# Performance work log

Measured on AMD Instinct MI355X. Metric: run time of the kernel, lower is better.

## Reference

```python
import jax, jax.numpy as jnp
import numpy as np
from jax import lax

HID, PROJ, DYN = 256, 256, 64
HW, BS, NQ = 6400, 16, 100


def setup_inputs() -> dict:
    key = jax.random.key(0)
    ks = jax.random.split(key, 10)
    p = lambda k, shape: jax.random.normal(k, shape, jnp.float32) * 0.02
    return {
        "query_feat": jax.random.normal(ks[0], (HW, BS, HID), jnp.float32),
        "support_feat": jax.random.normal(ks[1], (NQ, BS, HID), jnp.float32),
        "h": 80,
        "w": 80,
        "Wq": p(ks[2], (HID, PROJ)), "bq": jnp.zeros((PROJ,), jnp.float32),
        "Ws": p(ks[3], (HID, PROJ)), "bsp": jnp.zeros((PROJ,), jnp.float32),
        "W1": p(ks[4], (PROJ, DYN)), "b1": jnp.zeros((DYN,), jnp.float32),
        "W2": p(ks[5], (DYN, HID)), "b2": jnp.zeros((HID,), jnp.float32),
    }


def reference(query_feat, support_feat, h, w, Wq, bq, Ws, bsp, W1, b1, W2, b2):
    # query_feat: [hw, bs, c] -> [bs, hw, c]; support_feat: [nq, bs, c] -> [bs, nq, c]
    qf = jnp.transpose(query_feat, (1, 0, 2))
    sf = jnp.transpose(support_feat, (1, 0, 2))
    bsz, nq = sf.shape[0], sf.shape[1]
    hw = h * w

    fs_proj = sf @ Ws + bsp                      # [bs, nq, proj]
    fq_proj = qf @ Wq + bq                       # [bs, hw, proj]
    pattern = jnp.tanh(jax.nn.relu(fs_proj @ W1 + b1) @ W2 + b2)
    fs_feat = (pattern + 1.0) * fs_proj          # [bs, nq, proj]

    # bmm(fq, fs^T).T -> [bs, nq, hw]
    sim = jnp.einsum("bkp,bnp->bnk", fq_proj, fs_feat)
    similarity = sim.reshape(bsz, nq, h, w)

    # coordinate grid: x varies along w, y along h; flattened [hw, 2]
    gy = jnp.arange(h, dtype=jnp.float32) + 0.5
    gx = jnp.arange(w, dtype=jnp.float32) + 0.5
    X, Y = jnp.meshgrid(gx, gy, indexing="xy")  # each [h, w]
    coord = jnp.stack([X, Y], axis=-1).reshape(hw, 2)
    side = jnp.array([w, h], dtype=jnp.float32)

    sm = jax.nn.softmax(sim, axis=-1)            # [bs, nq, hw]
    proposal_for_loss = jnp.einsum("bnk,kd->bnd", sm, coord) / side

    # argmax peak -> one-hot -> 3x3 max-pool dilation (note (w,h) reshape per original)
    max_pos = jnp.argmax(sim, axis=-1)           # [bs, nq]
    max_mask = jax.nn.one_hot(max_pos, hw, dtype=jnp.float32).reshape(bsz, nq, w, h)
    local_mask = lax.reduce_window(
        max_mask, -jnp.inf, lax.max,
        window_dimensions=(1, 1, 3, 3), window_strides=(1, 1, 1, 1),
        padding=[(0, 0), (0, 0), (1, 1), (1, 1)],
    ).reshape(bsz, nq, hw)

    local_sm = sm * local_mask
    local_sm = local_sm / (jnp.sum(local_sm, axis=-1, keepdims=True) + 1e-10)
    proposals = jnp.einsum("bnk,kd->bnd", local_sm, coord) / side

    return proposal_for_loss, similarity, proposals
```

## Files before the change

kernel.cpp:

```cpp
#include <hip/hip_runtime.h>

#define HID 256
#define PROJ 256
#define DYN 64
#define HWD 6400
#define BSZ 16
#define NQ 100
#define HH 80
#define WW 80

typedef unsigned short u16;
typedef u16 u16x8 __attribute__((ext_vector_type(8)));
typedef __bf16 bf16x8 __attribute__((ext_vector_type(8)));
typedef float f32x4 __attribute__((ext_vector_type(4)));

__device__ __forceinline__ float bf2f(u16 h) {
    union { unsigned u; float f; } c; c.u = ((unsigned)h) << 16; return c.f;
}
__device__ __forceinline__ u16 f2bf(float f) {
    union { float f; unsigned u; } c; c.f = f;
    return (u16)((c.u + 0x7FFFu + ((c.u >> 16) & 1u)) >> 16);
}

__global__ __launch_bounds__(256, 1) void kpre(
    const float* __restrict__ support,
    const float* __restrict__ Wq, const float* __restrict__ bq,
    const float* __restrict__ Ws, const float* __restrict__ bsp,
    const float* __restrict__ W1, const float* __restrict__ b1,
    const float* __restrict__ W2, const float* __restrict__ b2,
    u16* __restrict__ pack, float* __restrict__ cvec)
{
    const int c = blockIdx.x;
    const int b = blockIdx.y;
    const int t = threadIdx.x;
    const int wv = t >> 6, lane = t & 63;

    __shared__ __align__(16) float sf_t[HID][8];
    __shared__ __align__(16) float fsp[8][PROJ];
    __shared__ __align__(16) float hid[8][DYN];
    __shared__ __align__(16) float fsf_t[PROJ][8];
    __shared__ float cacc[8][4];

    {
        const int nl = t >> 5;
        const int i0 = (t & 31) * 8;
        const int n = c * 8 + nl;
        float v[8];
        if (n < NQ) {
            const float* sp = support + (size_t)n * (BSZ * HID) + (size_t)b * HID + i0;
            const f32x4 a = *reinterpret_cast<const f32x4*>(sp);
            const f32x4 bb = *reinterpret_cast<const f32x4*>(sp + 4);
            v[0]=a[0]; v[1]=a[1]; v[2]=a[2]; v[3]=a[3];
            v[4]=bb[0]; v[5]=bb[1]; v[6]=bb[2]; v[7]=bb[3];
        } else {
            #pragma unroll
            for (int j = 0; j < 8; ++j) v[j] = 0.f;
        }
        #pragma unroll
        for (int j = 0; j < 8; ++j) sf_t[i0 + j][nl] = v[j];
    }
    __syncthreads();

    {
        const int p = t;
        float acc[8];
        #pragma unroll
        for (int n = 0; n < 8; ++n) acc[n] = 0.f;
        for (int i0 = 0; i0 < HID; i0 += 8) {
            float w[8];
            #pragma unroll
            for (int j = 0; j < 8; ++j) w[j] = Ws[(size_t)(i0 + j) * PROJ + p];
            #pragma unroll
            for (int j = 0; j < 8; ++j) {
                const f32x4 s0 = *reinterpret_cast<const f32x4*>(&sf_t[i0 + j][0]);
                const f32x4 s1 = *reinterpret_cast<const f32x4*>(&sf_t[i0 + j][4]);
                acc[0] += s0[0] * w[j]; acc[1] += s0[1] * w[j];
                acc[2] += s0[2] * w[j]; acc[3] += s0[3] * w[j];
                acc[4] += s1[0] * w[j]; acc[5] += s1[1] * w[j];
                acc[6] += s1[2] * w[j]; acc[7] += s1[3] * w[j];
            }
        }
        const float bb = bsp[p];
        #pragma unroll
        for (int n = 0; n < 8; ++n) fsp[n][p] = acc[n] + bb;
    }
    __syncthreads();

    {
        const int d = lane;
        #pragma unroll
        for (int pass = 0; pass < 2; ++pass) {
            const int nl = pass * 4 + wv;
            float a = 0.f;
            for (int p0 = 0; p0 < PROJ; p0 += 8) {
                float w[8];
                #pragma unroll
                for (int j = 0; j < 8; ++j) w[j] = W1[(size_t)(p0 + j) * DYN + d];
                #pragma unroll
                for (int j = 0; j < 8; ++j) a += fsp[nl][p0 + j] * w[j];
            }
            a += b1[d];
            hid[nl][d] = a > 0.f ? a : 0.f;
        }
    }
    __syncthreads();

    float cp[8];
    {
        const int p = t;
        const float bqv = bq[p];
        const float b2v = b2[p];
        float w[8][8];
        #pragma unroll
        for (int d0 = 0; d0 < 8; ++d0)
            #pragma unroll
            for (int j = 0; j < 8; ++j) w[d0][j] = W2[(size_t)(d0 * 8 + j) * PROJ + p];
        #pragma unroll
        for (int nl = 0; nl < 8; ++nl) {
            float a = 0.f;
            #pragma unroll
            for (int d0 = 0; d0 < 8; ++d0)
                #pragma unroll
                for (int j = 0; j < 8; ++j) a += hid[nl][d0 * 8 + j] * w[d0][j];
            const float pat = tanhf(a + b2v);
            const float ff = (pat + 1.f) * fsp[nl][p];
            fsf_t[p][nl] = ff;
            cp[nl] = bqv * ff;
        }
    }
    __syncthreads();

    #pragma unroll
    for (int nl = 0; nl < 8; ++nl) {
        float v = cp[nl];
        for (int off = 32; off > 0; off >>= 1) v += __shfl_down(v, off);
        if (lane == 0) cacc[nl][wv] = v;
    }
    __syncthreads();
    if (t < 8) {
        const int n = c * 8 + t;
        if (n < NQ) cvec[b * NQ + n] = cacc[t][0] + cacc[t][1] + cacc[t][2] + cacc[t][3];
    }

    {
        const int h = t;
        float acc[8];
        #pragma unroll
        for (int n = 0; n < 8; ++n) acc[n] = 0.f;
        for (int p0 = 0; p0 < PROJ; p0 += 8) {
            const float* wp = Wq + (size_t)h * PROJ + p0;
            const f32x4 w0 = *reinterpret_cast<const f32x4*>(wp);
            const f32x4 w1 = *reinterpret_cast<const f32x4*>(wp + 4);
            float wv8[8] = {w0[0], w0[1], w0[2], w0[3], w1[0], w1[1], w1[2], w1[3]};
            #pragma unroll
            for (int j = 0; j < 8; ++j) {
                const float w = wv8[j];
                const f32x4 f0 = *reinterpret_cast<const f32x4*>(&fsf_t[p0 + j][0]);
                const f32x4 f1 = *reinterpret_cast<const f32x4*>(&fsf_t[p0 + j][4]);
                acc[0] += f0[0] * w; acc[1] += f0[1] * w;
                acc[2] += f0[2] * w; acc[3] += f0[3] * w;
                acc[4] += f1[0] * w; acc[5] += f1[1] * w;
                acc[6] += f1[2] * w; acc[7] += f1[3] * w;
            }
        }
        const int ks = h >> 5, quad = (h >> 3) & 3, j = h & 7;
        const int nt = c >> 1;
        #pragma unroll
        for (int nl = 0; nl < 8; ++nl) {
            const int n = c * 8 + nl;
            const float f = (n < NQ) ? acc[nl] : 0.f;
            const u16 hi = f2bf(f);
            const u16 lo = f2bf(f - bf2f(hi));
            const int nit = (c & 1) * 8 + nl;
            const int lane2 = quad * 16 + nit;
            const size_t base = ((((size_t)b * 2 + 0) * 8 + ks) * 8 + nt) * 512 + lane2 * 8 + j;
            const size_t baseL = base + (size_t)8 * 8 * 512;
            pack[base] = hi;
            pack[baseL] = lo;
        }
    }
}

__global__ __launch_bounds__(256, 4) void ksim(
    const float* __restrict__ qf,
    const u16* __restrict__ pack,
    const float* __restrict__ cvec,
    float* __restrict__ sim)
{
    const int mc = blockIdx.x;
    const int b  = blockIdx.y;
    const int wv = threadIdx.x >> 6;
    const int lane = threadIdx.x & 63;
    const int quad = lane >> 4, l16 = lane & 15;

    f32x4 acc[7];
    #pragma unroll
    for (int nt = 0; nt < 7; ++nt) acc[nt] = (f32x4){0.f, 0.f, 0.f, 0.f};

    const int row = mc * 64 + wv * 16 + l16;
    const float* ap = qf + (size_t)row * (BSZ * HID) + b * HID + quad * 8;
    const u16* pb = pack + (size_t)b * (2 * 8 * 8 * 64 * 8) + (size_t)lane * 8;

    f32x4 a0 = *reinterpret_cast<const f32x4*>(ap + 0);
    f32x4 a1 = *reinterpret_cast<const f32x4*>(ap + 4);

    #pragma unroll
    for (int ks = 0; ks < 8; ++ks) {
        u16x8 uh[7], ul[7];
        #pragma unroll
        for (int nt = 0; nt < 7; ++nt) {
            uh[nt] = *reinterpret_cast<const u16x8*>(pb + ((size_t)(0 * 8 + ks) * 8 + nt) * 512);
            ul[nt] = *reinterpret_cast<const u16x8*>(pb + ((size_t)(1 * 8 + ks) * 8 + nt) * 512);
        }
        f32x4 n0, n1;
        if (ks < 7) {
            n0 = *reinterpret_cast<const f32x4*>(ap + (ks + 1) * 32 + 0);
            n1 = *reinterpret_cast<const f32x4*>(ap + (ks + 1) * 32 + 4);
        }
        bf16x8 ahi, alo;
        #pragma unroll
        for (int j = 0; j < 4; ++j) {
            const float v = a0[j];
            const __bf16 h = (__bf16)v;
            ahi[j] = h; alo[j] = (__bf16)(v - (float)h);
        }
        #pragma unroll
        for (int j = 0; j < 4; ++j) {
            const float v = a1[j];
            const __bf16 h = (__bf16)v;
            ahi[4 + j] = h; alo[4 + j] = (__bf16)(v - (float)h);
        }
        #pragma unroll
        for (int nt = 0; nt < 7; ++nt) {
            const bf16x8 bh = __builtin_bit_cast(bf16x8, uh[nt]);
            const bf16x8 bl = __builtin_bit_cast(bf16x8, ul[nt]);
            acc[nt] = __builtin_amdgcn_mfma_f32_16x16x32_bf16(ahi, bh, acc[nt], 0, 0, 0);
            acc[nt] = __builtin_amdgcn_mfma_f32_16x16x32_bf16(ahi, bl, acc[nt], 0, 0, 0);
            acc[nt] = __builtin_amdgcn_mfma_f32_16x16x32_bf16(alo, bh, acc[nt], 0, 0, 0);
        }
        a0 = n0; a1 = n1;
    }

    const int kbase = mc * 64 + wv * 16 + quad * 4;
    #pragma unroll
    for (int nt = 0; nt < 7; ++nt) {
        const int n = nt * 16 + l16;
        if (n >= NQ) continue;
        const float cadd = cvec[b * NQ + n];
        f32x4 o = acc[nt];
        o[0] += cadd; o[1] += cadd; o[2] += cadd; o[3] += cadd;
        *reinterpret_cast<f32x4*>(sim + (size_t)(b * NQ + n) * HWD + kbase) = o;
    }
}

__global__ __launch_bounds__(64, 4) void kfin(
    const float* __restrict__ sim,
    float* __restrict__ out)
{
    const int bn = blockIdx.x;
    const int lane = threadIdx.x;
    const float* src = sim + (size_t)bn * HWD;

    f32x4 v[25];
    #pragma unroll
    for (int j = 0; j < 25; ++j)
        v[j] = *reinterpret_cast<const f32x4*>(src + j * 256 + lane * 4);

    float bv = -3.4e38f; int bi = 0;
    #pragma unroll
    for (int j = 0; j < 25; ++j) {
        #pragma unroll
        for (int k = 0; k < 4; ++k) {
            if (v[j][k] > bv) { bv = v[j][k]; bi = j * 256 + lane * 4 + k; }
        }
    }
    #pragma unroll
    for (int m = 1; m < 64; m <<= 1) {
        const float ov = __shfl_xor(bv, m);
        const int oi = __shfl_xor(bi, m);
        if (ov > bv || (ov == bv && oi < bi)) { bv = ov; bi = oi; }
    }
    const int xc = bi % WW, yc = bi / WW;

    float s1 = 0.f, sx = 0.f, sy = 0.f;
    float wl = 0.f, wx = 0.f, wyv = 0.f;
    int x = (lane * 4) % WW, y = (lane * 4) / WW;
    #pragma unroll
    for (int j = 0; j < 25; ++j) {
        #pragma unroll
        for (int k = 0; k < 4; ++k) {
            int xe = x + k, ye = y;
            if (xe >= WW) { xe -= WW; ye += 1; }
            const float e = __expf(v[j][k] - bv);
            const float fx = (float)xe + 0.5f;
            const float fy = (float)ye + 0.5f;
            s1 += e; sx += e * fx; sy += e * fy;
            const int dx = xe - xc, dy = ye - yc;
            const bool inw = (dx >= -1 && dx <= 1 && dy >= -1 && dy <= 1);
            const float ew = inw ? e : 0.f;
            wl += ew; wx += ew * fx; wyv += ew * fy;
        }
        x += 16; y += 3;
        if (x >= WW) { x -= WW; y += 1; }
    }
    #pragma unroll
    for (int m = 1; m < 64; m <<= 1) {
        s1 += __shfl_xor(s1, m);
        sx += __shfl_xor(sx, m);
        sy += __shfl_xor(sy, m);
        wl += __shfl_xor(wl, m);
        wx += __shfl_xor(wx, m);
        wyv += __shfl_xor(wyv, m);
    }

    if (lane == 0) {
        const float invS = 1.f / s1;
        out[(size_t)bn * 2 + 0] = sx * invS / (float)WW;
        out[(size_t)bn * 2 + 1] = sy * invS / (float)HH;
        const float den = wl + 1e-10f * s1;
        const size_t pbase = 3200 + (size_t)BSZ * NQ * HWD;
        out[pbase + (size_t)bn * 2 + 0] = wx / den / (float)WW;
        out[pbase + (size_t)bn * 2 + 1] = wyv / den / (float)HH;
    }
}

extern "C" void kernel_launch(void* const* d_in, const int* in_sizes, int n_in,
                              void* d_out, int out_size, void* d_ws, size_t ws_size,
                              hipStream_t stream) {
    const float* qf  = (const float*)d_in[0];
    const float* sf  = (const float*)d_in[1];
    const float* Wq  = (const float*)d_in[4];
    const float* bq  = (const float*)d_in[5];
    const float* Ws  = (const float*)d_in[6];
    const float* bsp = (const float*)d_in[7];
    const float* W1  = (const float*)d_in[8];
    const float* b1  = (const float*)d_in[9];
    const float* W2  = (const float*)d_in[10];
    const float* b2  = (const float*)d_in[11];

    u16*   pack  = (u16*)d_ws;
    float* cvec  = (float*)((char*)d_ws + 2097152);
    float* out   = (float*)d_out;
    float* sim   = out + 3200;

    kpre<<<dim3(16, 16), 256, 0, stream>>>(sf, Wq, bq, Ws, bsp, W1, b1, W2, b2, pack, cvec);
    ksim<<<dim3(100, 16), 256, 0, stream>>>(qf, pack, cvec, sim);
    kfin<<<1600, 64, 0, stream>>>(sim, out);
}
```

Measured before the change: 275.1 us.

## Split kpre reductions across 1024 threads with shared-memory partial sums

The preprocessing kernel grows from 256 to 1024 threads per block. Each of the Ws projection, W1 hidden layer, W2 pattern and Wq fold stages is split along its reduction dimension across thread groups, with partial sums combined in shared memory. The grid drops from 16 to 14 column chunks, which still covers all 100 queries. The aim is to shorten the long serial, latency-bound per-thread loops in this small prologue kernel, at the cost of more shared memory, extra barriers and higher register pressure from the larger unrolled weight loads.

```diff
diff --git a/kernel.cpp b/kernel.cpp
--- a/kernel.cpp
+++ b/kernel.cpp
@@ -22,7 +22,7 @@
     return (u16)((c.u + 0x7FFFu + ((c.u >> 16) & 1u)) >> 16);
 }
 
-__global__ __launch_bounds__(256, 1) void kpre(
+__global__ __launch_bounds__(1024, 1) void kpre(
     const float* __restrict__ support,
     const float* __restrict__ Wq, const float* __restrict__ bq,
     const float* __restrict__ Ws, const float* __restrict__ bsp,
@@ -33,108 +33,126 @@
     const int c = blockIdx.x;
     const int b = blockIdx.y;
     const int t = threadIdx.x;
-    const int wv = t >> 6, lane = t & 63;
 
     __shared__ __align__(16) float sf_t[HID][8];
+    __shared__ __align__(16) float part[4][8][256];
     __shared__ __align__(16) float fsp[8][PROJ];
+    __shared__ __align__(16) float hidp[2][8][DYN];
     __shared__ __align__(16) float hid[8][DYN];
     __shared__ __align__(16) float fsf_t[PROJ][8];
     __shared__ float cacc[8][4];
 
-    {
-        const int nl = t >> 5;
-        const int i0 = (t & 31) * 8;
+    const int g = t >> 8;
+    const int p = t & 255;
+
+    {
+        const int nl = t >> 7;
+        const int i0 = (t & 127) * 2;
         const int n = c * 8 + nl;
-        float v[8];
+        float v0 = 0.f, v1 = 0.f;
         if (n < NQ) {
             const float* sp = support + (size_t)n * (BSZ * HID) + (size_t)b * HID + i0;
-            const f32x4 a = *reinterpret_cast<const f32x4*>(sp);
-            const f32x4 bb = *reinterpret_cast<const f32x4*>(sp + 4);
-            v[0]=a[0]; v[1]=a[1]; v[2]=a[2]; v[3]=a[3];
-            v[4]=bb[0]; v[5]=bb[1]; v[6]=bb[2]; v[7]=bb[3];
-        } else {
-            #pragma unroll
-            for (int j = 0; j < 8; ++j) v[j] = 0.f;
-        }
-        #pragma unroll
-        for (int j = 0; j < 8; ++j) sf_t[i0 + j][nl] = v[j];
-    }
-    __syncthreads();
-
-    {
-        const int p = t;
+            const float2 a = *reinterpret_cast<const float2*>(sp);
+            v0 = a.x; v1 = a.y;
+        }
+        sf_t[i0][nl] = v0;
+        sf_t[i0 + 1][nl] = v1;
+    }
+    __syncthreads();
+
+    {
         float acc[8];
         #pragma unroll
         for (int n = 0; n < 8; ++n) acc[n] = 0.f;
-        for (int i0 = 0; i0 < HID; i0 += 8) {
-            float w[8];
-            #pragma unroll
-            for (int j = 0; j < 8; ++j) w[j] = Ws[(size_t)(i0 + j) * PROJ + p];
-            #pragma unroll
-            for (int j = 0; j < 8; ++j) {
-                const f32x4 s0 = *reinterpret_cast<const f32x4*>(&sf_t[i0 + j][0]);
-                const f32x4 s1 = *reinterpret_cast<const f32x4*>(&sf_t[i0 + j][4]);
+        const int ibase = g * 64;
+        #pragma unroll
+        for (int ib = 0; ib < 64; ib += 32) {
+            float w[32];
+            #pragma unroll
+            for (int j = 0; j < 32; ++j)
+                w[j] = Ws[(size_t)(ibase + ib + j) * PROJ + p];
+            #pragma unroll
+            for (int j = 0; j < 32; ++j) {
+                const f32x4 s0 = *reinterpret_cast<const f32x4*>(&sf_t[ibase + ib + j][0]);
+                const f32x4 s1 = *reinterpret_cast<const f32x4*>(&sf_t[ibase + ib + j][4]);
                 acc[0] += s0[0] * w[j]; acc[1] += s0[1] * w[j];
                 acc[2] += s0[2] * w[j]; acc[3] += s0[3] * w[j];
                 acc[4] += s1[0] * w[j]; acc[5] += s1[1] * w[j];
                 acc[6] += s1[2] * w[j]; acc[7] += s1[3] * w[j];
             }
         }
+        #pragma unroll
+        for (int n = 0; n < 8; ++n) part[g][n][p] = acc[n];
+    }
+    __syncthreads();
+    {
+        const int na = t >> 8;
         const float bb = bsp[p];
         #pragma unroll
-        for (int n = 0; n < 8; ++n) fsp[n][p] = acc[n] + bb;
-    }
-    __syncthreads();
-
-    {
-        const int d = lane;
-        #pragma unroll
-        for (int pass = 0; pass < 2; ++pass) {
-            const int nl = pass * 4 + wv;
-            float a = 0.f;
-            for (int p0 = 0; p0 < PROJ; p0 += 8) {
-                float w[8];
-                #pragma unroll
-                for (int j = 0; j < 8; ++j) w[j] = W1[(size_t)(p0 + j) * DYN + d];
-                #pragma unroll
-                for (int j = 0; j < 8; ++j) a += fsp[nl][p0 + j] * w[j];
+        for (int k = 0; k < 2; ++k) {
+            const int n = na + k * 4;
+            fsp[n][p] = part[0][n][p] + part[1][n][p] + part[2][n][p] + part[3][n][p] + bb;
+        }
+    }
+    __syncthreads();
+
+    {
+        const int ph = t >> 9;
+        const int n = (t >> 6) & 7;
+        const int d = t & 63;
+        float a = 0.f;
+        const int pb0 = ph * 128;
+        #pragma unroll
+        for (int pb = 0; pb < 128; pb += 32) {
+            float w[32];
+            #pragma unroll
+            for (int j = 0; j < 32; ++j)
+                w[j] = W1[(size_t)(pb0 + pb + j) * DYN + d];
+            #pragma unroll
+            for (int j = 0; j < 32; j += 4) {
+                const f32x4 s = *reinterpret_cast<const f32x4*>(&fsp[n][pb0 + pb + j]);
+                a += s[0] * w[j] + s[1] * w[j + 1] + s[2] * w[j + 2] + s[3] * w[j + 3];
             }
-            a += b1[d];
-            hid[nl][d] = a > 0.f ? a : 0.f;
-        }
-    }
-    __syncthreads();
-
-    float cp[8];
-    {
-        const int p = t;
+        }
+        hidp[ph][n][d] = a;
+    }
+    __syncthreads();
+    if (t < 512) {
+        const int n = t >> 6, d = t & 63;
+        const float a = hidp[0][n][d] + hidp[1][n][d] + b1[d];
+        hid[n][d] = a > 0.f ? a : 0.f;
+    }
+    __syncthreads();
+
+    {
+        const int nh = t >> 8;
+        const int n0 = nh * 2, n1 = nh * 2 + 1;
         const float bqv = bq[p];
         const float b2v = b2[p];
-        float w[8][8];
-        #pragma unroll
-        for (int d0 = 0; d0 < 8; ++d0)
-            #pragma unroll
-            for (int j = 0; j < 8; ++j) w[d0][j] = W2[(size_t)(d0 * 8 + j) * PROJ + p];
-        #pragma unroll
-        for (int nl = 0; nl < 8; ++nl) {
-            float a = 0.f;
-            #pragma unroll
-            for (int d0 = 0; d0 < 8; ++d0)
-                #pragma unroll
-                for (int j = 0; j < 8; ++j) a += hid[nl][d0 * 8 + j] * w[d0][j];
-            const float pat = tanhf(a + b2v);
-            const float ff = (pat + 1.f) * fsp[nl][p];
-            fsf_t[p][nl] = ff;
-            cp[nl] = bqv * ff;
-        }
-    }
-    __syncthreads();
-
-    #pragma unroll
-    for (int nl = 0; nl < 8; ++nl) {
-        float v = cp[nl];
-        for (int off = 32; off > 0; off >>= 1) v += __shfl_down(v, off);
-        if (lane == 0) cacc[nl][wv] = v;
+        float w[64];
+        #pragma unroll
+        for (int d = 0; d < 64; ++d) w[d] = W2[(size_t)d * PROJ + p];
+        float a0 = 0.f, a1 = 0.f;
+        #pragma unroll
+        for (int d0 = 0; d0 < 64; d0 += 4) {
+            const f32x4 h0 = *reinterpret_cast<const f32x4*>(&hid[n0][d0]);
+            const f32x4 h1 = *reinterpret_cast<const f32x4*>(&hid[n1][d0]);
+            a0 += h0[0] * w[d0] + h0[1] * w[d0 + 1] + h0[2] * w[d0 + 2] + h0[3] * w[d0 + 3];
+            a1 += h1[0] * w[d0] + h1[1] * w[d0 + 1] + h1[2] * w[d0 + 2] + h1[3] * w[d0 + 3];
+        }
+        const float pat0 = tanhf(a0 + b2v);
+        const float pat1 = tanhf(a1 + b2v);
+        const float ff0 = (pat0 + 1.f) * fsp[n0][p];
+        const float ff1 = (pat1 + 1.f) * fsp[n1][p];
+        *reinterpret_cast<float2*>(&fsf_t[p][n0]) = make_float2(ff0, ff1);
+        float cp0 = bqv * ff0, cp1 = bqv * ff1;
+        for (int off = 32; off > 0; off >>= 1) {
+            cp0 += __shfl_down(cp0, off);
+            cp1 += __shfl_down(cp1, off);
+        }
+        const int lane = t & 63;
+        const int ps = (t >> 6) & 3;
+        if (lane == 0) { cacc[n0][ps] = cp0; cacc[n1][ps] = cp1; }
     }
     __syncthreads();
     if (t < 8) {
@@ -143,40 +161,55 @@
     }
 
     {
-        const int h = t;
+        const int h = p;
         float acc[8];
         #pragma unroll
         for (int n = 0; n < 8; ++n) acc[n] = 0.f;
-        for (int p0 = 0; p0 < PROJ; p0 += 8) {
-            const float* wp = Wq + (size_t)h * PROJ + p0;
-            const f32x4 w0 = *reinterpret_cast<const f32x4*>(wp);
-            const f32x4 w1 = *reinterpret_cast<const f32x4*>(wp + 4);
-            float wv8[8] = {w0[0], w0[1], w0[2], w0[3], w1[0], w1[1], w1[2], w1[3]};
-            #pragma unroll
-            for (int j = 0; j < 8; ++j) {
-                const float w = wv8[j];
-                const f32x4 f0 = *reinterpret_cast<const f32x4*>(&fsf_t[p0 + j][0]);
-                const f32x4 f1 = *reinterpret_cast<const f32x4*>(&fsf_t[p0 + j][4]);
-                acc[0] += f0[0] * w; acc[1] += f0[1] * w;
-                acc[2] += f0[2] * w; acc[3] += f0[3] * w;
-                acc[4] += f1[0] * w; acc[5] += f1[1] * w;
-                acc[6] += f1[2] * w; acc[7] += f1[3] * w;
+        const int pbase = g * 64;
+        #pragma unroll
+        for (int pb = 0; pb < 64; pb += 32) {
+            f32x4 wv4[8];
+            #pragma unroll
+            for (int k = 0; k < 8; ++k)
+                wv4[k] = *reinterpret_cast<const f32x4*>(Wq + (size_t)h * PROJ + pbase + pb + k * 4);
+            #pragma unroll
+            for (int k = 0; k < 8; ++k) {
+                #pragma unroll
+                for (int m = 0; m < 4; ++m) {
+                    const int pp = pbase + pb + k * 4 + m;
+                    const float w = wv4[k][m];
+                    const f32x4 f0 = *reinterpret_cast<const f32x4*>(&fsf_t[pp][0]);
+                    const f32x4 f1 = *reinterpret_cast<const f32x4*>(&fsf_t[pp][4]);
+                    acc[0] += f0[0] * w; acc[1] += f0[1] * w;
+                    acc[2] += f0[2] * w; acc[3] += f0[3] * w;
+                    acc[4] += f1[0] * w; acc[5] += f1[1] * w;
+                    acc[6] += f1[2] * w; acc[7] += f1[3] * w;
+                }
             }
         }
+        #pragma unroll
+        for (int n = 0; n < 8; ++n) part[g][n][h] = acc[n];
+    }
+    __syncthreads();
+
+    {
+        const int h = p;
+        const int na = t >> 8;
         const int ks = h >> 5, quad = (h >> 3) & 3, j = h & 7;
         const int nt = c >> 1;
         #pragma unroll
-        for (int nl = 0; nl < 8; ++nl) {
+        for (int k = 0; k < 2; ++k) {
+            const int nl = na + k * 4;
             const int n = c * 8 + nl;
-            const float f = (n < NQ) ? acc[nl] : 0.f;
+            float f = part[0][nl][h] + part[1][nl][h] + part[2][nl][h] + part[3][nl][h];
+            if (n >= NQ) f = 0.f;
             const u16 hi = f2bf(f);
             const u16 lo = f2bf(f - bf2f(hi));
             const int nit = (c & 1) * 8 + nl;
             const int lane2 = quad * 16 + nit;
             const size_t base = ((((size_t)b * 2 + 0) * 8 + ks) * 8 + nt) * 512 + lane2 * 8 + j;
-            const size_t baseL = base + (size_t)8 * 8 * 512;
             pack[base] = hi;
-            pack[baseL] = lo;
+            pack[base + (size_t)8 * 8 * 512] = lo;
         }
     }
 }
@@ -343,7 +376,7 @@
     float* out   = (float*)d_out;
     float* sim   = out + 3200;
 
-    kpre<<<dim3(16, 16), 256, 0, stream>>>(sf, Wq, bq, Ws, bsp, W1, b1, W2, b2, pack, cvec);
+    kpre<<<dim3(14, 16), 1024, 0, stream>>>(sf, Wq, bq, Ws, bsp, W1, b1, W2, b2, pack, cvec);
     ksim<<<dim3(100, 16), 256, 0, stream>>>(qf, pack, cvec, sim);
     kfin<<<1600, 64, 0, stream>>>(sim, out);
 }
```

Result: no change. 271.6 us (-1.3%).
